# Optimization experiments

Hardware: AMD Instinct MI355X
Metric: run time of the kernel (lower is better)

Reference implementation:

```python
import jax, jax.numpy as jnp
from jax import lax
import numpy as np

B, T, H = 128, 512, 512  # batch, seq_length, hidden_dim (== input_dim)


def _xavier(key, shape):
    fan_in, fan_out = shape[1], shape[0]
    limit = float(np.sqrt(6.0 / (fan_in + fan_out)))
    return jax.random.uniform(key, shape, jnp.float32, -limit, limit)


def setup_inputs() -> dict:
    key = jax.random.key(0)
    ks = jax.random.split(key, 10)
    s = 1.0 / np.sqrt(H)  # torch LSTM default init range
    return {
        "x": jax.random.normal(ks[0], (B, T, H), jnp.float32),
        "W_ih": jax.random.uniform(ks[1], (4 * H, H), jnp.float32, -s, s),
        "W_hh": jax.random.uniform(ks[2], (4 * H, H), jnp.float32, -s, s),
        "b_ih": jax.random.uniform(ks[3], (4 * H,), jnp.float32, -s, s),
        "b_hh": jax.random.uniform(ks[4], (4 * H,), jnp.float32, -s, s),
        "Ve": _xavier(ks[5], (1, H)),
        "U1": _xavier(ks[6], (H, 2 * H)),
        "U2": _xavier(ks[7], (H, H)),
        "W_out": _xavier(ks[8], (2, H)),
        "b_out": jnp.zeros((2,), jnp.float32),
    }


def _lstm(x, W_ih, W_hh, b_ih, b_hh):
    # x: [B, T, D] -> hidden states [B, T, H]; PyTorch gate order i,f,g,o
    b = b_ih + b_hh
    # precompute input projections for all timesteps: [T, B, 4H]
    xg = jnp.einsum('btd,gd->tbg', x, W_ih) + b

    def step(carry, xt):
        h, c = carry
        g = xt + h @ W_hh.T  # [B, 4H]
        i, f, gg, o = jnp.split(g, 4, axis=1)
        c = jax.nn.sigmoid(f) * c + jax.nn.sigmoid(i) * jnp.tanh(gg)
        h = jax.nn.sigmoid(o) * jnp.tanh(c)
        return (h, c), h

    h0 = jnp.zeros((x.shape[0], W_hh.shape[1]), x.dtype)
    (_, _), hs = lax.scan(step, (h0, h0), xg)
    return jnp.swapaxes(hs, 0, 1)  # [B, T, H]


def reference(x, W_ih, W_hh, b_ih, b_hh, Ve, U1, U2, W_out, b_out):
    h = _lstm(x, W_ih, W_hh, b_ih, b_hh)  # [B, T, H]
    h_last = h[:, -1, :]  # [B, H]
    # additive attention, vectorized over all timesteps
    Hdim = h.shape[-1]
    u1 = jnp.einsum('bth,gh->btg', h, U1[:, :Hdim]) + jnp.einsum('bh,gh->bg', h_last, U1[:, Hdim:])[:, None, :]
    u2 = jnp.einsum('btd,gd->btg', x, U2)
    u = jnp.tanh(u1 + u2)  # [B, T, H]
    e = jnp.einsum('bth,h->bt', u, Ve[0])
    alpha = jax.nn.softmax(e, axis=1)  # [B, T]
    context = jnp.einsum('bt,bth->bh', alpha, h)  # [B, H]
    params = context @ W_out.T + b_out  # [B, 2]
    mu = params[:, 0]
    sigma = jax.nn.softplus(params[:, 1]) + 1e-5
    return (mu, sigma)
```

## Files before the change

kernel.cpp:

```cpp
#include <hip/hip_runtime.h>
#include <stdint.h>


using short8  = __attribute__((ext_vector_type(8))) short;
using short4v = __attribute__((ext_vector_type(4))) short;
using floatx4 = __attribute__((ext_vector_type(4))) float;

#define MFMA16(a, b, c) __builtin_amdgcn_mfma_f32_16x16x32_bf16((a), (b), (c), 0, 0, 0)

__device__ __forceinline__ unsigned short f2b(float f) {
    unsigned u = __float_as_uint(f);
    u += 0x7FFFu + ((u >> 16) & 1u);
    return (unsigned short)(u >> 16);
}
__device__ __forceinline__ float b2f(unsigned short h) {
    return __uint_as_float(((unsigned)h) << 16);
}
__device__ __forceinline__ float sigm(float x) { return 1.0f / (1.0f + __expf(-x)); }
__device__ __forceinline__ float tanh_(float x) { return 1.0f - 2.0f / (__expf(2.0f * x) + 1.0f); }

__global__ __launch_bounds__(256) void prep(
    const float* __restrict__ x, const float* __restrict__ Wih, const float* __restrict__ Whh,
    const float* __restrict__ bih, const float* __restrict__ bhh,
    const float* __restrict__ U1, const float* __restrict__ U2,
    unsigned short* __restrict__ x_bf, unsigned short* __restrict__ Wih_bf,
    unsigned short* __restrict__ Whh_bf, unsigned short* __restrict__ U1a,
    unsigned short* __restrict__ U1b, unsigned short* __restrict__ U2b,
    float* __restrict__ bias)
{
    const long long NX4 = 33554432LL / 4;
    const long long NREST = 1048576LL + 1048576LL + 524288LL + 262144LL + 2048LL;
    const long long total = NX4 + NREST;
    for (long long u = (long long)blockIdx.x * 256 + threadIdx.x; u < total;
         u += (long long)gridDim.x * 256) {
        if (u < NX4) {
            float4 v = ((const float4*)x)[u];
            short4v o;
            o[0] = (short)f2b(v.x); o[1] = (short)f2b(v.y);
            o[2] = (short)f2b(v.z); o[3] = (short)f2b(v.w);
            *(short4v*)&x_bf[u * 4] = o;
        } else {
            long long i = u - NX4;
            if (i < 1048576) { Wih_bf[i] = f2b(Wih[i]); continue; }
            i -= 1048576;
            if (i < 1048576) { Whh_bf[i] = f2b(Whh[i]); continue; }
            i -= 1048576;
            if (i < 524288) {
                int row = (int)(i >> 10), col = (int)(i & 1023);
                if (col < 512) U1a[row * 512 + col] = f2b(U1[i]);
                else           U1b[row * 512 + (col - 512)] = f2b(U1[i]);
                continue;
            }
            i -= 524288;
            if (i < 262144) { U2b[i] = f2b(U2[i]); continue; }
            i -= 262144;
            bias[i] = bih[i] + bhh[i];
        }
    }
}

__device__ __forceinline__ void gemm_core(
    const unsigned short* __restrict__ A, long long lda,
    const unsigned short* __restrict__ Bm, long long ldb,
    unsigned short* __restrict__ C, long long ldc,
    const float* __restrict__ bias, int mode,
    int m0, int n0, int tid, unsigned short* sbuf)
{
    unsigned short* At = sbuf;
    unsigned short* Bt = sbuf + 128 * 72;
    unsigned short* Ct = sbuf;

    const int wv = tid >> 6, lane = tid & 63, l15 = lane & 15, q = lane >> 4;
    const int wm = wv & 1, wn = wv >> 1;

    floatx4 acc[4][4];
    for (int i = 0; i < 4; i++)
        for (int j = 0; j < 4; j++) acc[i][j] = (floatx4){0.f, 0.f, 0.f, 0.f};

    for (int k0 = 0; k0 < 512; k0 += 64) {
        for (int p = 0; p < 4; p++) {
            int idx = tid + p * 256;
            int row = idx >> 3, ch = idx & 7;
            *(short8*)&At[row * 72 + ch * 8] =
                *(const short8*)&A[(long long)(m0 + row) * lda + k0 + ch * 8];
            *(short8*)&Bt[row * 72 + ch * 8] =
                *(const short8*)&Bm[(long long)(n0 + row) * ldb + k0 + ch * 8];
        }
        __syncthreads();
        for (int ks = 0; ks < 64; ks += 32) {
            short8 af[4], bfv[4];
            for (int mi = 0; mi < 4; mi++)
                af[mi] = *(const short8*)&At[(wm * 64 + mi * 16 + l15) * 72 + ks + q * 8];
            for (int ni = 0; ni < 4; ni++)
                bfv[ni] = *(const short8*)&Bt[(wn * 64 + ni * 16 + l15) * 72 + ks + q * 8];
            for (int mi = 0; mi < 4; mi++)
                for (int ni = 0; ni < 4; ni++)
                    acc[mi][ni] = MFMA16(af[mi], bfv[ni], acc[mi][ni]);
        }
        __syncthreads();
    }

    float bv[4];
    for (int ni = 0; ni < 4; ni++)
        bv[ni] = bias ? bias[n0 + wn * 64 + ni * 16 + l15] : 0.0f;

    for (int mi = 0; mi < 4; mi++)
        for (int ni = 0; ni < 4; ni++)
            for (int r = 0; r < 4; r++)
                Ct[(wm * 64 + mi * 16 + q * 4 + r) * 128 + wn * 64 + ni * 16 + l15] =
                    f2b(acc[mi][ni][r] + bv[ni]);
    __syncthreads();

    const int tt0 = m0 & 511, bglob = m0 >> 9;
    for (int p = 0; p < 8; p++) {
        int idx = tid + p * 256;
        int row = idx >> 4, ch = idx & 15;
        if (mode) {
            int n = n0 + ch * 8;
            int gate = n >> 9, jg = (n >> 4) & 31, c0 = gate * 16 + (n & 15);
            long long dst = (((long long)(tt0 + row) * 32 + jg) * 128 + bglob) * 64 + c0;
            *(short8*)&C[dst] = *(const short8*)&Ct[row * 128 + ch * 8];
        } else {
            *(short8*)&C[(long long)(m0 + row) * ldc + n0 + ch * 8] =
                *(const short8*)&Ct[row * 128 + ch * 8];
        }
    }
}

__global__ __launch_bounds__(256) void gemm_bt(
    const unsigned short* __restrict__ A, long long lda,
    const unsigned short* __restrict__ Bm, long long ldb,
    unsigned short* __restrict__ C, long long ldc,
    const float* __restrict__ bias, int mode, int mmul)
{
    __shared__ __align__(16) unsigned short sbuf[2 * 128 * 72];
    gemm_core(A, lda, Bm, ldb, C, ldc, bias, mode,
              blockIdx.x * mmul, blockIdx.y * 128, threadIdx.x, sbuf);
}

#define GEMM_WGS 6144
#define ATTN_WGS 2048
__global__ __launch_bounds__(256, 1) void mega(
    const unsigned short* __restrict__ xg,
    const unsigned short* __restrict__ Whh,
    unsigned short* __restrict__ h_all,
    unsigned int* __restrict__ ring,
    const unsigned short* __restrict__ x_bf,
    const unsigned short* __restrict__ Wih_bf,
    const float* __restrict__ bias,
    unsigned short* __restrict__ xg_out,
    int* __restrict__ syncp,
    const unsigned short* __restrict__ U1a,
    const unsigned short* __restrict__ U2b)
{
    __shared__ __align__(16) char smem[86016];

    const int tid = threadIdx.x;

    if (blockIdx.x >= 64 && blockIdx.x < 64 + GEMM_WGS) {
        int g = blockIdx.x - 64;
        int b = g & 127;
        int r = g >> 7;
        int ti = 1 + (r % 3);
        int n = r / 3;
        gemm_core(x_bf, 512, Wih_bf, 512, xg_out, 2048, bias, 1,
                  b * 512 + ti * 128, n * 128, tid, (unsigned short*)smem);
        __syncthreads();
        if (tid == 0)
            __hip_atomic_fetch_add(&syncp[0], 1, __ATOMIC_RELEASE,
                                   __HIP_MEMORY_SCOPE_AGENT);
        return;
    }

    if (blockIdx.x >= 64 + GEMM_WGS) {
        const int g = blockIdx.x - 64 - GEMM_WGS;
        const int tt = g >> 7;
        const int b  = g & 127;
        const int t0 = tt * 32;
        const int bg = b >> 4;

        if (tid < 8) {
            while (__hip_atomic_load(&syncp[16 + (bg * 8 + tid) * 16],
                                     __ATOMIC_RELAXED,
                                     __HIP_MEMORY_SCOPE_AGENT) < t0 + 32)
                __builtin_amdgcn_s_sleep(8);
        }
        __syncthreads();

        unsigned short* Bt2 = (unsigned short*)smem;
        unsigned short* At2 = (unsigned short*)smem + 512 * 40;

        const int wv = tid >> 6, lane = tid & 63, l15 = lane & 15, q = lane >> 4;

        floatx4 acc[2][8];
        for (int mi = 0; mi < 2; mi++)
            for (int ni = 0; ni < 8; ni++) acc[mi][ni] = (floatx4){0.f, 0.f, 0.f, 0.f};

        for (int it = 0; it < 32; it++) {
            const int phase = it >> 4, kk = (it & 15) * 32;
            const unsigned short* Bsrc = phase ? U2b : U1a;
            __syncthreads();
            for (int idx = tid; idx < 2048; idx += 256) {
                int row = idx >> 2, ch = idx & 3;
                *(short8*)&Bt2[row * 40 + ch * 8] =
                    *(const short8*)&Bsrc[(long long)row * 512 + kk + ch * 8];
            }
            if (tid < 128) {
                int row = tid >> 2, ch = tid & 3;
                if (phase == 0) {
                    unsigned long long* p = (unsigned long long*)
                        &h_all[((long long)b * 512 + t0 + row) * 512 + kk + ch * 8];
                    unsigned long long lo = __hip_atomic_load(p, __ATOMIC_RELAXED,
                                                              __HIP_MEMORY_SCOPE_AGENT);
                    unsigned long long hi = __hip_atomic_load(p + 1, __ATOMIC_RELAXED,
                                                              __HIP_MEMORY_SCOPE_AGENT);
                    unsigned long long* d = (unsigned long long*)&At2[row * 40 + ch * 8];
                    d[0] = lo; d[1] = hi;
                } else {
                    *(short8*)&At2[row * 40 + ch * 8] =
                        *(const short8*)&x_bf[((long long)b * 512 + t0 + row) * 512 + kk + ch * 8];
                }
            }
            __syncthreads();
            short8 af0 = *(const short8*)&At2[(l15) * 40 + q * 8];
            short8 af1 = *(const short8*)&At2[(16 + l15) * 40 + q * 8];
            for (int ni = 0; ni < 8; ni++) {
                short8 bfv = *(const short8*)&Bt2[(wv * 128 + ni * 16 + l15) * 40 + q * 8];
                acc[0][ni] = MFMA16(af0, bfv, acc[0][ni]);
                acc[1][ni] = MFMA16(af1, bfv, acc[1][ni]);
            }
        }
        for (int mi = 0; mi < 2; mi++)
            for (int ni = 0; ni < 8; ni++) {
                const int n = wv * 128 + ni * 16 + l15;
                #pragma unroll
                for (int r = 0; r < 4; r++) {
                    const int t = t0 + mi * 16 + q * 4 + r;
                    float* slot = (float*)&xg_out[(((long long)t * 32 + (n >> 5)) * 128 + b) * 64];
                    slot[n & 31] = acc[mi][ni][r];
                }
            }
        return;
    }

    unsigned int (*At)[16 * 264] = (unsigned int (*)[16 * 264])smem;

    const int wv = tid >> 6, lane = tid & 63, l15 = lane & 15, q = lane >> 4;
    const int bg = blockIdx.x >> 3, jgb = blockIdx.x & 7;
    const int b0 = bg * 16;
    const int jg32 = jgb * 4 + wv;
    const int hid = jg32 * 16 + l15;

    short8 Wreg[4][16];
    #pragma unroll
    for (int ct = 0; ct < 4; ct++)
        #pragma unroll
        for (int kk = 0; kk < 16; kk++)
            Wreg[ct][kk] = *(const short8*)
                &Whh[(long long)(ct * 512 + hid) * 512 + kk * 32 + q * 8];

    float cst[4] = {0.f, 0.f, 0.f, 0.f};

    for (int t = 0; t < 512; t++) {
        if (t == 128) {
            if (tid == 0) {
                while (__hip_atomic_load(&syncp[0], __ATOMIC_ACQUIRE,
                                         __HIP_MEMORY_SCOPE_AGENT) < GEMM_WGS)
                    __builtin_amdgcn_s_sleep(8);
            }
            __syncthreads();
        }
        const long long xbase = ((long long)(t * 32 + jg32) * 128 + b0) * 64;
        floatx4 acc[4];
        #pragma unroll
        for (int ct = 0; ct < 4; ct++)
            #pragma unroll
            for (int r = 0; r < 4; r++)
                acc[ct][r] = b2f(xg[xbase + (q * 4 + r) * 64 + ct * 16 + l15]);

        if (t > 0) {
            const unsigned want = (unsigned)(t - 1);
            const int sl = (t - 1) & 1;
            unsigned long long* rb = (unsigned long long*)
                (ring + sl * 65536 + b0 * 512);
            unsigned long long w[16];
            #pragma unroll
            for (int i = 0; i < 16; i++)
                w[i] = __hip_atomic_load(&rb[tid + i * 256], __ATOMIC_RELAXED,
                                         __HIP_MEMORY_SCOPE_AGENT);
            while (true) {
                unsigned bad = 0;
                #pragma unroll
                for (int i = 0; i < 16; i++) {
                    unsigned lo = (unsigned)(w[i] >> 16) & 0xFFFFu;
                    unsigned hi = (unsigned)(w[i] >> 48);
                    bad |= (lo ^ want) | (hi ^ want);
                }
                if (!bad) break;
                #pragma unroll
                for (int i = 0; i < 16; i++) {
                    unsigned lo = (unsigned)(w[i] >> 16) & 0xFFFFu;
                    unsigned hi = (unsigned)(w[i] >> 48);
                    if ((lo ^ want) | (hi ^ want))
                        w[i] = __hip_atomic_load(&rb[tid + i * 256], __ATOMIC_RELAXED,
                                                 __HIP_MEMORY_SCOPE_AGENT);
                }
            }
            unsigned int* dst = &At[sl][0];
            #pragma unroll
            for (int i = 0; i < 16; i++) {
                int idx = tid + i * 256;
                int row = idx >> 8, k = idx & 255;
                dst[row * 264 + k] =
                    (unsigned)(w[i] & 0xFFFFu) | ((unsigned)(w[i] >> 32) << 16);
            }
            __syncthreads();
            const unsigned int* ap = &At[sl][l15 * 264 + q * 4];
            #pragma unroll
            for (int kk = 0; kk < 16; kk++) {
                short8 af = *(const short8*)(ap + kk * 16);
                acc[0] = MFMA16(af, Wreg[0][kk], acc[0]);
                acc[1] = MFMA16(af, Wreg[1][kk], acc[1]);
                acc[2] = MFMA16(af, Wreg[2][kk], acc[2]);
                acc[3] = MFMA16(af, Wreg[3][kk], acc[3]);
            }
        }
        unsigned short hbv[4];
        #pragma unroll
        for (int r = 0; r < 4; r++) {
            float ig = sigm(acc[0][r]);
            float fg = sigm(acc[1][r]);
            float gv = tanh_(acc[2][r]);
            float og = sigm(acc[3][r]);
            cst[r] = fg * cst[r] + ig * gv;
            hbv[r] = f2b(og * tanh_(cst[r]));
        }
        #pragma unroll
        for (int r = 0; r < 4; r++) {
            const int b = b0 + q * 4 + r;
            __hip_atomic_store(&ring[(t & 1) * 65536 + b * 512 + hid],
                               ((unsigned)t << 16) | hbv[r], __ATOMIC_RELAXED,
                               __HIP_MEMORY_SCOPE_AGENT);
        }
        #pragma unroll
        for (int r = 0; r < 4; r++) {
            const int b = b0 + q * 4 + r;
            int o = __shfl_xor((int)hbv[r], 1);
            if (!(l15 & 1)) {
                unsigned v = (unsigned)hbv[r] | (((unsigned)(unsigned short)o) << 16);
                __hip_atomic_store(
                    (unsigned*)&h_all[(long long)b * 262144 + (long long)t * 512 + hid],
                    v, __ATOMIC_RELAXED, __HIP_MEMORY_SCOPE_AGENT);
            }
        }
        if ((t & 15) == 15) {
            __syncthreads();
            if (tid == 0)
                __hip_atomic_store(&syncp[16 + (int)blockIdx.x * 16], t + 1,
                                   __ATOMIC_RELAXED, __HIP_MEMORY_SCOPE_AGENT);
        }
    }
}

__global__ __launch_bounds__(256) void attn_out(
    const unsigned short* __restrict__ a_xg,
    const unsigned short* __restrict__ h_all,
    const unsigned short* __restrict__ u1bv,
    const float* __restrict__ Ve,
    const float* __restrict__ Wout, const float* __restrict__ bout,
    float* __restrict__ outp)
{
    __shared__ float se[512];
    __shared__ float sm[512];
    __shared__ float red[8];
    const int b = blockIdx.x, tid = threadIdx.x;
    const int wv = tid >> 6, lane = tid & 63;

    const int n0 = lane * 8;
    float ve[8], ub[8];
    #pragma unroll
    for (int j = 0; j < 8; j++) {
        ve[j] = Ve[n0 + j];
        ub[j] = b2f(u1bv[b * 512 + n0 + j]);
    }
    for (int it = 0; it < 64; it++) {
        const int t = it * 8 + wv * 2;
        const float* s0p = (const float*)
            &a_xg[(((long long)t * 32 + (n0 >> 5)) * 128 + b) * 64];
        const float* s1p = (const float*)
            &a_xg[(((long long)(t + 1) * 32 + (n0 >> 5)) * 128 + b) * 64];
        float4 a0 = *(const float4*)&s0p[n0 & 31];
        float4 a1 = *(const float4*)&s0p[(n0 & 31) + 4];
        float4 a2 = *(const float4*)&s1p[n0 & 31];
        float4 a3 = *(const float4*)&s1p[(n0 & 31) + 4];
        float s0 = ve[0] * tanh_(a0.x + ub[0]) + ve[1] * tanh_(a0.y + ub[1])
                 + ve[2] * tanh_(a0.z + ub[2]) + ve[3] * tanh_(a0.w + ub[3])
                 + ve[4] * tanh_(a1.x + ub[4]) + ve[5] * tanh_(a1.y + ub[5])
                 + ve[6] * tanh_(a1.z + ub[6]) + ve[7] * tanh_(a1.w + ub[7]);
        float s1 = ve[0] * tanh_(a2.x + ub[0]) + ve[1] * tanh_(a2.y + ub[1])
                 + ve[2] * tanh_(a2.z + ub[2]) + ve[3] * tanh_(a2.w + ub[3])
                 + ve[4] * tanh_(a3.x + ub[4]) + ve[5] * tanh_(a3.y + ub[5])
                 + ve[6] * tanh_(a3.z + ub[6]) + ve[7] * tanh_(a3.w + ub[7]);
        #pragma unroll
        for (int off = 1; off <= 32; off <<= 1) {
            s0 += __shfl_xor(s0, off);
            s1 += __shfl_xor(s1, off);
        }
        if (lane == 0) { se[t] = s0; se[t + 1] = s1; }
    }
    __syncthreads();

    float e0 = se[tid], e1 = se[256 + tid];
    float mx = fmaxf(e0, e1);
    for (int off = 32; off; off >>= 1) mx = fmaxf(mx, __shfl_xor(mx, off));
    if (lane == 0) red[wv] = mx;
    __syncthreads();
    mx = fmaxf(fmaxf(red[0], red[1]), fmaxf(red[2], red[3]));

    float s0 = __expf(e0 - mx), s1 = __expf(e1 - mx);
    sm[tid] = s0; sm[256 + tid] = s1;
    float ss = s0 + s1;
    for (int off = 32; off; off >>= 1) ss += __shfl_xor(ss, off);
    if (lane == 0) red[4 + wv] = ss;
    __syncthreads();
    float inv = 1.0f / (red[4] + red[5] + red[6] + red[7]);

    const unsigned int* hp = (const unsigned int*)(h_all + (long long)b * 262144);
    float a0 = 0.f, a1 = 0.f;
    for (int t = 0; t < 512; t += 4) {
        #pragma unroll
        for (int j = 0; j < 4; j++) {
            float al = sm[t + j];
            unsigned v = hp[(t + j) * 256 + tid];
            a0 += al * b2f((unsigned short)(v & 0xFFFFu));
            a1 += al * b2f((unsigned short)(v >> 16));
        }
    }
    a0 *= inv; a1 *= inv;

    float q0 = a0 * Wout[2 * tid] + a1 * Wout[2 * tid + 1];
    float q1 = a0 * Wout[512 + 2 * tid] + a1 * Wout[512 + 2 * tid + 1];
    for (int off = 32; off; off >>= 1) { q0 += __shfl_xor(q0, off); q1 += __shfl_xor(q1, off); }
    __syncthreads();
    if (lane == 0) { red[wv] = q0; red[4 + wv] = q1; }
    __syncthreads();
    if (tid == 0) {
        float P0 = red[0] + red[1] + red[2] + red[3] + bout[0];
        float P1 = red[4] + red[5] + red[6] + red[7] + bout[1];
        outp[b] = P0;
        float sp = (P1 > 15.0f) ? P1 : log1pf(__expf(P1));
        outp[128 + b] = sp + 1e-5f;
    }
}

extern "C" void kernel_launch(void* const* d_in, const int* in_sizes, int n_in,
                              void* d_out, int out_size, void* d_ws, size_t ws_size,
                              hipStream_t stream)
{
    const float* x    = (const float*)d_in[0];
    const float* Wih  = (const float*)d_in[1];
    const float* Whh  = (const float*)d_in[2];
    const float* bih  = (const float*)d_in[3];
    const float* bhh  = (const float*)d_in[4];
    const float* Ve   = (const float*)d_in[5];
    const float* U1   = (const float*)d_in[6];
    const float* U2   = (const float*)d_in[7];
    const float* Wout = (const float*)d_in[8];
    const float* bout = (const float*)d_in[9];
    float* out = (float*)d_out;

    char* ws = (char*)d_ws;
    size_t off = 0;
    auto alloc = [&](size_t bytes) -> void* {
        void* p = ws + off;
        off += (bytes + 255) & ~(size_t)255;
        return p;
    };
    unsigned short* x_bf   = (unsigned short*)alloc(33554432ull * 2);
    unsigned short* Wih_bf = (unsigned short*)alloc(1048576ull * 2);
    unsigned short* Whh_bf = (unsigned short*)alloc(1048576ull * 2);
    unsigned short* U1a    = (unsigned short*)alloc(262144ull * 2);
    unsigned short* U1b    = (unsigned short*)alloc(262144ull * 2);
    unsigned short* U2b    = (unsigned short*)alloc(262144ull * 2);
    float*          bias   = (float*)alloc(2048ull * 4);
    unsigned short* xg     = (unsigned short*)alloc(134217728ull * 2);
    unsigned short* h_all  = (unsigned short*)alloc(33554432ull * 2);
    unsigned short* u1bv   = (unsigned short*)alloc(65536ull * 2);
    unsigned int*   ring   = (unsigned int*)alloc(131072ull * 4);
    int*            syncp  = (int*)alloc(8192ull);
    if (off > ws_size) return;

    hipMemsetAsync(syncp, 0, 8192, stream);
    prep<<<4096, 256, 0, stream>>>(x, Wih, Whh, bih, bhh, U1, U2,
                                   x_bf, Wih_bf, Whh_bf, U1a, U1b, U2b, bias);
    gemm_bt<<<dim3(128, 16), 256, 0, stream>>>(x_bf, 512, Wih_bf, 512,
                                               xg, 2048, bias, 1, 512);
    mega<<<64 + GEMM_WGS + ATTN_WGS, 256, 0, stream>>>(
        xg, Whh_bf, h_all, ring, x_bf, Wih_bf, bias, xg, syncp, U1a, U2b);
    gemm_bt<<<dim3(1, 4), 256, 0, stream>>>(h_all + 511 * 512, 262144, U1b, 512,
                                            u1bv, 512, nullptr, 0, 128);
    attn_out<<<128, 256, 0, stream>>>(xg, h_all, u1bv, Ve, Wout, bout, out);
}
```

Before: 2.562 ms.

## Fuse input-projection GEMM into mega kernel with per-timestep readiness flags

Removes the separate upfront input-projection GEMM launch and instead computes all of xg inside the persistent mega kernel, with one workgroup per (timestep, 128-column tile). Each tile bumps a per-timestep counter that the recurrent blocks poll every 16 steps, so the recurrence can start as soon as early timesteps are ready. The last attention chunk is split into narrower column tiles so it finishes sooner after the recurrence ends. The small h_last·U1b GEMM is folded into attn_out, which drops a launch. The risk is that GEMM workgroups contend with the latency-bound recurrent blocks for CUs and bandwidth, and each block now reads the full K=512 of a 128-row batch slice for a single timestep.

```diff
diff --git a/kernel.cpp b/kernel.cpp
--- a/kernel.cpp
+++ b/kernel.cpp
@@ -59,12 +59,12 @@
     }
 }
 
-__device__ __forceinline__ void gemm_core(
+__device__ __forceinline__ void gemm_core_t(
     const unsigned short* __restrict__ A, long long lda,
-    const unsigned short* __restrict__ Bm, long long ldb,
-    unsigned short* __restrict__ C, long long ldc,
-    const float* __restrict__ bias, int mode,
-    int m0, int n0, int tid, unsigned short* sbuf)
+    const unsigned short* __restrict__ Bm,
+    unsigned short* __restrict__ C,
+    const float* __restrict__ bias,
+    int n0, int tfix, int tid, unsigned short* sbuf)
 {
     unsigned short* At = sbuf;
     unsigned short* Bt = sbuf + 128 * 72;
@@ -82,9 +82,9 @@
             int idx = tid + p * 256;
             int row = idx >> 3, ch = idx & 7;
             *(short8*)&At[row * 72 + ch * 8] =
-                *(const short8*)&A[(long long)(m0 + row) * lda + k0 + ch * 8];
+                *(const short8*)&A[(long long)row * lda + k0 + ch * 8];
             *(short8*)&Bt[row * 72 + ch * 8] =
-                *(const short8*)&Bm[(long long)(n0 + row) * ldb + k0 + ch * 8];
+                *(const short8*)&Bm[(long long)(n0 + row) * 512 + k0 + ch * 8];
         }
         __syncthreads();
         for (int ks = 0; ks < 64; ks += 32) {
@@ -102,7 +102,7 @@
 
     float bv[4];
     for (int ni = 0; ni < 4; ni++)
-        bv[ni] = bias ? bias[n0 + wn * 64 + ni * 16 + l15] : 0.0f;
+        bv[ni] = bias[n0 + wn * 64 + ni * 16 + l15];
 
     for (int mi = 0; mi < 4; mi++)
         for (int ni = 0; ni < 4; ni++)
@@ -111,35 +111,99 @@
                     f2b(acc[mi][ni][r] + bv[ni]);
     __syncthreads();
 
-    const int tt0 = m0 & 511, bglob = m0 >> 9;
     for (int p = 0; p < 8; p++) {
         int idx = tid + p * 256;
         int row = idx >> 4, ch = idx & 15;
-        if (mode) {
-            int n = n0 + ch * 8;
-            int gate = n >> 9, jg = (n >> 4) & 31, c0 = gate * 16 + (n & 15);
-            long long dst = (((long long)(tt0 + row) * 32 + jg) * 128 + bglob) * 64 + c0;
-            *(short8*)&C[dst] = *(const short8*)&Ct[row * 128 + ch * 8];
-        } else {
-            *(short8*)&C[(long long)(m0 + row) * ldc + n0 + ch * 8] =
-                *(const short8*)&Ct[row * 128 + ch * 8];
-        }
-    }
-}
-
-__global__ __launch_bounds__(256) void gemm_bt(
-    const unsigned short* __restrict__ A, long long lda,
-    const unsigned short* __restrict__ Bm, long long ldb,
-    unsigned short* __restrict__ C, long long ldc,
-    const float* __restrict__ bias, int mode, int mmul)
+        int n = n0 + ch * 8;
+        int gate = n >> 9, jg = (n >> 4) & 31, c0 = gate * 16 + (n & 15);
+        long long dst = (((long long)tfix * 32 + jg) * 128 + row) * 64 + c0;
+        *(short8*)&C[dst] = *(const short8*)&Ct[row * 128 + ch * 8];
+    }
+}
+
+template<int NNI>
+__device__ __forceinline__ void attn_helper_body(
+    const unsigned short* __restrict__ h_all,
+    const unsigned short* __restrict__ x_bf,
+    const unsigned short* __restrict__ U1a,
+    const unsigned short* __restrict__ U2b,
+    unsigned short* __restrict__ xg_out,
+    int* __restrict__ syncp,
+    int b, int t0, int nBase, int tid, char* smem)
 {
-    __shared__ __align__(16) unsigned short sbuf[2 * 128 * 72];
-    gemm_core(A, lda, Bm, ldb, C, ldc, bias, mode,
-              blockIdx.x * mmul, blockIdx.y * 128, threadIdx.x, sbuf);
-}
-
-#define GEMM_WGS 6144
-#define ATTN_WGS 2048
+    const int bg = b >> 4;
+    if (tid < 8) {
+        while (__hip_atomic_load(&syncp[16 + (bg * 8 + tid) * 16],
+                                 __ATOMIC_RELAXED,
+                                 __HIP_MEMORY_SCOPE_AGENT) < t0 + 32)
+            __builtin_amdgcn_s_sleep(8);
+    }
+    __syncthreads();
+
+    unsigned short* Bt2 = (unsigned short*)smem;
+    unsigned short* At2 = (unsigned short*)smem + (NNI * 64) * 40;
+
+    const int wv = tid >> 6, lane = tid & 63, l15 = lane & 15, q = lane >> 4;
+
+    floatx4 acc[2][NNI];
+    #pragma unroll
+    for (int mi = 0; mi < 2; mi++)
+        #pragma unroll
+        for (int ni = 0; ni < NNI; ni++) acc[mi][ni] = (floatx4){0.f, 0.f, 0.f, 0.f};
+
+    for (int it = 0; it < 32; it++) {
+        const int phase = it >> 4, kk = (it & 15) * 32;
+        const unsigned short* Bsrc = phase ? U2b : U1a;
+        __syncthreads();
+        #pragma unroll
+        for (int pp = 0; pp < NNI; pp++) {
+            int idx = tid + pp * 256;
+            int row = idx >> 2, ch = idx & 3;
+            *(short8*)&Bt2[row * 40 + ch * 8] =
+                *(const short8*)&Bsrc[(long long)(nBase + row) * 512 + kk + ch * 8];
+        }
+        if (tid < 128) {
+            int row = tid >> 2, ch = tid & 3;
+            if (phase == 0) {
+                unsigned long long* p = (unsigned long long*)
+                    &h_all[((long long)b * 512 + t0 + row) * 512 + kk + ch * 8];
+                unsigned long long lo = __hip_atomic_load(p, __ATOMIC_RELAXED,
+                                                          __HIP_MEMORY_SCOPE_AGENT);
+                unsigned long long hi = __hip_atomic_load(p + 1, __ATOMIC_RELAXED,
+                                                          __HIP_MEMORY_SCOPE_AGENT);
+                unsigned long long* d = (unsigned long long*)&At2[row * 40 + ch * 8];
+                d[0] = lo; d[1] = hi;
+            } else {
+                *(short8*)&At2[row * 40 + ch * 8] =
+                    *(const short8*)&x_bf[((long long)b * 512 + t0 + row) * 512 + kk + ch * 8];
+            }
+        }
+        __syncthreads();
+        short8 af0 = *(const short8*)&At2[(l15) * 40 + q * 8];
+        short8 af1 = *(const short8*)&At2[(16 + l15) * 40 + q * 8];
+        #pragma unroll
+        for (int ni = 0; ni < NNI; ni++) {
+            short8 bfv = *(const short8*)&Bt2[(wv * (NNI * 16) + ni * 16 + l15) * 40 + q * 8];
+            acc[0][ni] = MFMA16(af0, bfv, acc[0][ni]);
+            acc[1][ni] = MFMA16(af1, bfv, acc[1][ni]);
+        }
+    }
+    #pragma unroll
+    for (int mi = 0; mi < 2; mi++)
+        #pragma unroll
+        for (int ni = 0; ni < NNI; ni++) {
+            const int n = nBase + wv * (NNI * 16) + ni * 16 + l15;
+            #pragma unroll
+            for (int r = 0; r < 4; r++) {
+                const int t = t0 + mi * 16 + q * 4 + r;
+                float* slot = (float*)&xg_out[(((long long)t * 32 + (n >> 5)) * 128 + b) * 64];
+                slot[n & 31] = acc[mi][ni][r];
+            }
+        }
+}
+
+#define GEMM_WGS 8192
+#define ATTN_WGS 2432
 __global__ __launch_bounds__(256, 1) void mega(
     const unsigned short* __restrict__ xg,
     const unsigned short* __restrict__ Whh,
@@ -159,87 +223,27 @@
 
     if (blockIdx.x >= 64 && blockIdx.x < 64 + GEMM_WGS) {
         int g = blockIdx.x - 64;
-        int b = g & 127;
-        int r = g >> 7;
-        int ti = 1 + (r % 3);
-        int n = r / 3;
-        gemm_core(x_bf, 512, Wih_bf, 512, xg_out, 2048, bias, 1,
-                  b * 512 + ti * 128, n * 128, tid, (unsigned short*)smem);
+        int t = g >> 4;
+        int n0 = (g & 15) << 7;
+        gemm_core_t(x_bf + (long long)t * 512, 512LL * 512, Wih_bf,
+                    xg_out, bias, n0, t, tid, (unsigned short*)smem);
         __syncthreads();
         if (tid == 0)
-            __hip_atomic_fetch_add(&syncp[0], 1, __ATOMIC_RELEASE,
+            __hip_atomic_fetch_add(&syncp[1088 + t], 1, __ATOMIC_RELEASE,
                                    __HIP_MEMORY_SCOPE_AGENT);
         return;
     }
 
     if (blockIdx.x >= 64 + GEMM_WGS) {
         const int g = blockIdx.x - 64 - GEMM_WGS;
-        const int tt = g >> 7;
-        const int b  = g & 127;
-        const int t0 = tt * 32;
-        const int bg = b >> 4;
-
-        if (tid < 8) {
-            while (__hip_atomic_load(&syncp[16 + (bg * 8 + tid) * 16],
-                                     __ATOMIC_RELAXED,
-                                     __HIP_MEMORY_SCOPE_AGENT) < t0 + 32)
-                __builtin_amdgcn_s_sleep(8);
-        }
-        __syncthreads();
-
-        unsigned short* Bt2 = (unsigned short*)smem;
-        unsigned short* At2 = (unsigned short*)smem + 512 * 40;
-
-        const int wv = tid >> 6, lane = tid & 63, l15 = lane & 15, q = lane >> 4;
-
-        floatx4 acc[2][8];
-        for (int mi = 0; mi < 2; mi++)
-            for (int ni = 0; ni < 8; ni++) acc[mi][ni] = (floatx4){0.f, 0.f, 0.f, 0.f};
-
-        for (int it = 0; it < 32; it++) {
-            const int phase = it >> 4, kk = (it & 15) * 32;
-            const unsigned short* Bsrc = phase ? U2b : U1a;
-            __syncthreads();
-            for (int idx = tid; idx < 2048; idx += 256) {
-                int row = idx >> 2, ch = idx & 3;
-                *(short8*)&Bt2[row * 40 + ch * 8] =
-                    *(const short8*)&Bsrc[(long long)row * 512 + kk + ch * 8];
-            }
-            if (tid < 128) {
-                int row = tid >> 2, ch = tid & 3;
-                if (phase == 0) {
-                    unsigned long long* p = (unsigned long long*)
-                        &h_all[((long long)b * 512 + t0 + row) * 512 + kk + ch * 8];
-                    unsigned long long lo = __hip_atomic_load(p, __ATOMIC_RELAXED,
-                                                              __HIP_MEMORY_SCOPE_AGENT);
-                    unsigned long long hi = __hip_atomic_load(p + 1, __ATOMIC_RELAXED,
-                                                              __HIP_MEMORY_SCOPE_AGENT);
-                    unsigned long long* d = (unsigned long long*)&At2[row * 40 + ch * 8];
-                    d[0] = lo; d[1] = hi;
-                } else {
-                    *(short8*)&At2[row * 40 + ch * 8] =
-                        *(const short8*)&x_bf[((long long)b * 512 + t0 + row) * 512 + kk + ch * 8];
-                }
-            }
-            __syncthreads();
-            short8 af0 = *(const short8*)&At2[(l15) * 40 + q * 8];
-            short8 af1 = *(const short8*)&At2[(16 + l15) * 40 + q * 8];
-            for (int ni = 0; ni < 8; ni++) {
-                short8 bfv = *(const short8*)&Bt2[(wv * 128 + ni * 16 + l15) * 40 + q * 8];
-                acc[0][ni] = MFMA16(af0, bfv, acc[0][ni]);
-                acc[1][ni] = MFMA16(af1, bfv, acc[1][ni]);
-            }
-        }
-        for (int mi = 0; mi < 2; mi++)
-            for (int ni = 0; ni < 8; ni++) {
-                const int n = wv * 128 + ni * 16 + l15;
-                #pragma unroll
-                for (int r = 0; r < 4; r++) {
-                    const int t = t0 + mi * 16 + q * 4 + r;
-                    float* slot = (float*)&xg_out[(((long long)t * 32 + (n >> 5)) * 128 + b) * 64];
-                    slot[n & 31] = acc[mi][ni][r];
-                }
-            }
+        if (g < 1920) {
+            attn_helper_body<8>(h_all, x_bf, U1a, U2b, xg_out, syncp,
+                                g & 127, (g >> 7) * 32, 0, tid, smem);
+        } else {
+            const int j = g - 1920;
+            attn_helper_body<2>(h_all, x_bf, U1a, U2b, xg_out, syncp,
+                                j & 127, 480, (j >> 7) * 128, tid, smem);
+        }
         return;
     }
 
@@ -262,10 +266,10 @@
     float cst[4] = {0.f, 0.f, 0.f, 0.f};
 
     for (int t = 0; t < 512; t++) {
-        if (t == 128) {
-            if (tid == 0) {
-                while (__hip_atomic_load(&syncp[0], __ATOMIC_ACQUIRE,
-                                         __HIP_MEMORY_SCOPE_AGENT) < GEMM_WGS)
+        if ((t & 15) == 0) {
+            if (tid < 16) {
+                while (__hip_atomic_load(&syncp[1088 + t + tid], __ATOMIC_ACQUIRE,
+                                         __HIP_MEMORY_SCOPE_AGENT) < 16)
                     __builtin_amdgcn_s_sleep(8);
             }
             __syncthreads();
@@ -365,23 +369,46 @@
 __global__ __launch_bounds__(256) void attn_out(
     const unsigned short* __restrict__ a_xg,
     const unsigned short* __restrict__ h_all,
-    const unsigned short* __restrict__ u1bv,
+    const unsigned short* __restrict__ U1b,
     const float* __restrict__ Ve,
     const float* __restrict__ Wout, const float* __restrict__ bout,
     float* __restrict__ outp)
 {
+    __shared__ float hl[512];
+    __shared__ float u1s[512];
     __shared__ float se[512];
     __shared__ float sm[512];
     __shared__ float red[8];
     const int b = blockIdx.x, tid = threadIdx.x;
     const int wv = tid >> 6, lane = tid & 63;
 
+    {
+        unsigned v = ((const unsigned*)(h_all + (long long)b * 262144 + 511LL * 512))[tid];
+        hl[2 * tid]     = b2f((unsigned short)(v & 0xFFFFu));
+        hl[2 * tid + 1] = b2f((unsigned short)(v >> 16));
+    }
+    __syncthreads();
+    #pragma unroll
+    for (int rr = 0; rr < 2; rr++) {
+        const int n = tid + rr * 256;
+        const unsigned short* up = &U1b[(long long)n * 512];
+        float s = 0.f;
+        for (int k = 0; k < 512; k += 8) {
+            short8 v8 = *(const short8*)&up[k];
+            #pragma unroll
+            for (int j = 0; j < 8; j++)
+                s += hl[k + j] * b2f((unsigned short)v8[j]);
+        }
+        u1s[n] = s;
+    }
+    __syncthreads();
+
     const int n0 = lane * 8;
     float ve[8], ub[8];
     #pragma unroll
     for (int j = 0; j < 8; j++) {
         ve[j] = Ve[n0 + j];
-        ub[j] = b2f(u1bv[b * 512 + n0 + j]);
+        ub[j] = u1s[n0 + j];
     }
     for (int it = 0; it < 64; it++) {
         const int t = it * 8 + wv * 2;
@@ -485,7 +512,6 @@
     float*          bias   = (float*)alloc(2048ull * 4);
     unsigned short* xg     = (unsigned short*)alloc(134217728ull * 2);
     unsigned short* h_all  = (unsigned short*)alloc(33554432ull * 2);
-    unsigned short* u1bv   = (unsigned short*)alloc(65536ull * 2);
     unsigned int*   ring   = (unsigned int*)alloc(131072ull * 4);
     int*            syncp  = (int*)alloc(8192ull);
     if (off > ws_size) return;
@@ -493,11 +519,7 @@
     hipMemsetAsync(syncp, 0, 8192, stream);
     prep<<<4096, 256, 0, stream>>>(x, Wih, Whh, bih, bhh, U1, U2,
                                    x_bf, Wih_bf, Whh_bf, U1a, U1b, U2b, bias);
-    gemm_bt<<<dim3(128, 16), 256, 0, stream>>>(x_bf, 512, Wih_bf, 512,
-                                               xg, 2048, bias, 1, 512);
     mega<<<64 + GEMM_WGS + ATTN_WGS, 256, 0, stream>>>(
         xg, Whh_bf, h_all, ring, x_bf, Wih_bf, bias, xg, syncp, U1a, U2b);
-    gemm_bt<<<dim3(1, 4), 256, 0, stream>>>(h_all + 511 * 512, 262144, U1b, 512,
-                                            u1bv, 512, nullptr, 0, 128);
-    attn_out<<<128, 256, 0, stream>>>(xg, h_all, u1bv, Ve, Wout, bout, out);
-}
+    attn_out<<<128, 256, 0, stream>>>(xg, h_all, U1b, Ve, Wout, bout, out);
+}
```

New measurement: 2.645 ms. 3.3% more time.

## Replace per-step barrier with split wave flags, prefetch ring, fuse u1b GEMV

Applied to the files above, without the earlier changes.

In the recurrent loop, the ring loads for step t-1 are now issued before the xg loads so their latency overlaps. The block-wide __syncthreads is replaced by per-wave LDS flags, which lets each wave start the first half of its K MFMAs once waves 0-1 have staged their rows. The LDS staging index is simplified to row i, column tid. Separately, the small h_last·U1b GEMM kernel launch is removed and its GEMV is folded into attn_out. This cuts one launch but adds a serial 512x512 dot-product loop per block.

```diff
diff --git a/kernel.cpp b/kernel.cpp
--- a/kernel.cpp
+++ b/kernel.cpp
@@ -154,6 +154,7 @@
     const unsigned short* __restrict__ U2b)
 {
     __shared__ __align__(16) char smem[86016];
+    __shared__ int wflag[2][4];
 
     const int tid = threadIdx.x;
 
@@ -251,6 +252,9 @@
     const int jg32 = jgb * 4 + wv;
     const int hid = jg32 * 16 + l15;
 
+    if (tid < 8) ((int*)wflag)[tid] = -1;
+    __syncthreads();
+
     short8 Wreg[4][16];
     #pragma unroll
     for (int ct = 0; ct < 4; ct++)
@@ -270,6 +274,19 @@
             }
             __syncthreads();
         }
+
+        const unsigned want = (unsigned)(t - 1);
+        const int sl = (t - 1) & 1;
+        unsigned long long* rb = (unsigned long long*)
+            (ring + sl * 65536 + b0 * 512);
+        unsigned long long w[16];
+        if (t > 0) {
+            #pragma unroll
+            for (int i = 0; i < 16; i++)
+                w[i] = __hip_atomic_load(&rb[tid + i * 256], __ATOMIC_RELAXED,
+                                         __HIP_MEMORY_SCOPE_AGENT);
+        }
+
         const long long xbase = ((long long)(t * 32 + jg32) * 128 + b0) * 64;
         floatx4 acc[4];
         #pragma unroll
@@ -279,15 +296,6 @@
                 acc[ct][r] = b2f(xg[xbase + (q * 4 + r) * 64 + ct * 16 + l15]);
 
         if (t > 0) {
-            const unsigned want = (unsigned)(t - 1);
-            const int sl = (t - 1) & 1;
-            unsigned long long* rb = (unsigned long long*)
-                (ring + sl * 65536 + b0 * 512);
-            unsigned long long w[16];
-            #pragma unroll
-            for (int i = 0; i < 16; i++)
-                w[i] = __hip_atomic_load(&rb[tid + i * 256], __ATOMIC_RELAXED,
-                                         __HIP_MEMORY_SCOPE_AGENT);
             while (true) {
                 unsigned bad = 0;
                 #pragma unroll
@@ -308,16 +316,30 @@
             }
             unsigned int* dst = &At[sl][0];
             #pragma unroll
-            for (int i = 0; i < 16; i++) {
-                int idx = tid + i * 256;
-                int row = idx >> 8, k = idx & 255;
-                dst[row * 264 + k] =
+            for (int i = 0; i < 16; i++)
+                dst[i * 264 + tid] =
                     (unsigned)(w[i] & 0xFFFFu) | ((unsigned)(w[i] >> 32) << 16);
-            }
-            __syncthreads();
+            __hip_atomic_store(&wflag[sl][wv], (int)want, __ATOMIC_RELEASE,
+                               __HIP_MEMORY_SCOPE_WORKGROUP);
+            while (__hip_atomic_load(&wflag[sl][0], __ATOMIC_ACQUIRE,
+                                     __HIP_MEMORY_SCOPE_WORKGROUP) != (int)want ||
+                   __hip_atomic_load(&wflag[sl][1], __ATOMIC_ACQUIRE,
+                                     __HIP_MEMORY_SCOPE_WORKGROUP) != (int)want) {}
             const unsigned int* ap = &At[sl][l15 * 264 + q * 4];
             #pragma unroll
-            for (int kk = 0; kk < 16; kk++) {
+            for (int kk = 0; kk < 8; kk++) {
+                short8 af = *(const short8*)(ap + kk * 16);
+                acc[0] = MFMA16(af, Wreg[0][kk], acc[0]);
+                acc[1] = MFMA16(af, Wreg[1][kk], acc[1]);
+                acc[2] = MFMA16(af, Wreg[2][kk], acc[2]);
+                acc[3] = MFMA16(af, Wreg[3][kk], acc[3]);
+            }
+            while (__hip_atomic_load(&wflag[sl][2], __ATOMIC_ACQUIRE,
+                                     __HIP_MEMORY_SCOPE_WORKGROUP) != (int)want ||
+                   __hip_atomic_load(&wflag[sl][3], __ATOMIC_ACQUIRE,
+                                     __HIP_MEMORY_SCOPE_WORKGROUP) != (int)want) {}
+            #pragma unroll
+            for (int kk = 8; kk < 16; kk++) {
                 short8 af = *(const short8*)(ap + kk * 16);
                 acc[0] = MFMA16(af, Wreg[0][kk], acc[0]);
                 acc[1] = MFMA16(af, Wreg[1][kk], acc[1]);
@@ -365,23 +387,46 @@
 __global__ __launch_bounds__(256) void attn_out(
     const unsigned short* __restrict__ a_xg,
     const unsigned short* __restrict__ h_all,
-    const unsigned short* __restrict__ u1bv,
+    const unsigned short* __restrict__ U1b,
     const float* __restrict__ Ve,
     const float* __restrict__ Wout, const float* __restrict__ bout,
     float* __restrict__ outp)
 {
+    __shared__ float hl[512];
+    __shared__ float u1s[512];
     __shared__ float se[512];
     __shared__ float sm[512];
     __shared__ float red[8];
     const int b = blockIdx.x, tid = threadIdx.x;
     const int wv = tid >> 6, lane = tid & 63;
 
+    {
+        unsigned v = ((const unsigned*)(h_all + (long long)b * 262144 + 511LL * 512))[tid];
+        hl[2 * tid]     = b2f((unsigned short)(v & 0xFFFFu));
+        hl[2 * tid + 1] = b2f((unsigned short)(v >> 16));
+    }
+    __syncthreads();
+    #pragma unroll
+    for (int rr = 0; rr < 2; rr++) {
+        const int n = tid + rr * 256;
+        const unsigned short* up = &U1b[(long long)n * 512];
+        float s = 0.f;
+        for (int k = 0; k < 512; k += 8) {
+            short8 v8 = *(const short8*)&up[k];
+            #pragma unroll
+            for (int j = 0; j < 8; j++)
+                s += hl[k + j] * b2f((unsigned short)v8[j]);
+        }
+        u1s[n] = s;
+    }
+    __syncthreads();
+
     const int n0 = lane * 8;
     float ve[8], ub[8];
     #pragma unroll
     for (int j = 0; j < 8; j++) {
         ve[j] = Ve[n0 + j];
-        ub[j] = b2f(u1bv[b * 512 + n0 + j]);
+        ub[j] = u1s[n0 + j];
     }
     for (int it = 0; it < 64; it++) {
         const int t = it * 8 + wv * 2;
@@ -485,7 +530,6 @@
     float*          bias   = (float*)alloc(2048ull * 4);
     unsigned short* xg     = (unsigned short*)alloc(134217728ull * 2);
     unsigned short* h_all  = (unsigned short*)alloc(33554432ull * 2);
-    unsigned short* u1bv   = (unsigned short*)alloc(65536ull * 2);
     unsigned int*   ring   = (unsigned int*)alloc(131072ull * 4);
     int*            syncp  = (int*)alloc(8192ull);
     if (off > ws_size) return;
@@ -497,7 +541,5 @@
                                                xg, 2048, bias, 1, 512);
     mega<<<64 + GEMM_WGS + ATTN_WGS, 256, 0, stream>>>(
         xg, Whh_bf, h_all, ring, x_bf, Wih_bf, bias, xg, syncp, U1a, U2b);
-    gemm_bt<<<dim3(1, 4), 256, 0, stream>>>(h_all + 511 * 512, 262144, U1b, 512,
-                                            u1bv, 512, nullptr, 0, 128);
-    attn_out<<<128, 256, 0, stream>>>(xg, h_all, u1bv, Ve, Wout, bout, out);
-}
+    attn_out<<<128, 256, 0, stream>>>(xg, h_all, U1b, Ve, Wout, bout, out);
+}
```

Measured after the change: 3.138 ms. +22.5%, slower.
